# Performance work log

Hardware: AMD Instinct MI355X
Metric: run time of the kernel (lower is better)

## Reference

```python
import jax, jax.numpy as jnp
import numpy as np

PI = 3.141592653589793


def setup_inputs() -> dict:
    key = jax.random.key(0)
    k1, k2, k3, k4 = jax.random.split(key, 4)
    B, N, C, H, V = 4, 4096, 128, 8, 16
    inputs = jax.random.normal(k1, (B, N, C), dtype=jnp.float32)
    dist = jax.random.uniform(k2, (N, N), dtype=jnp.float32)
    r = jax.random.normal(k3, (H, 1, 1), dtype=jnp.float32)
    weight = jax.random.normal(k4, (H, C, V), dtype=jnp.float32)
    return {"inputs": inputs, "dist": dist, "r": r, "weight": weight, "locality": 64}


def reference(inputs, dist, r, weight, locality):
    # scaled_dist: (H, N, N) -- learnable bandwidth per head via tan/sin transform
    scaled = dist[None, :, :] * jnp.tan(0.25 * PI * (1.0 + jnp.sin(r)))
    # quantile-based local masking along last axis (linear interpolation,
    # matching tfp.stats.percentile with interpolation='linear')
    mask = jnp.percentile(scaled, float(locality), axis=-1, keepdims=True, method="linear")
    fmax = jnp.finfo(jnp.float32).max
    scaled = jnp.where(scaled <= mask, scaled, fmax)
    # softmax over key axis of -scaled_dist (masked entries -> -fmax -> ~0 weight)
    att = jax.nn.softmax(-scaled, axis=-1)  # (H, N, N)
    # per-head value projection: (B,N,C) x (H,C,V) -> (B,H,N,V)
    value = jnp.einsum("bnj,hjk->bhnk", inputs, weight)
    # attention aggregation: (H,N,N) x (B,H,N,V) -> (B,H,N,V)
    concat = jnp.einsum("hnj,bhjd->bhnd", att, value)
    B, H, N, V = concat.shape
    concat = concat.transpose(0, 2, 1, 3).reshape(B, N, H * V)  # (B, N, hid_dim)
    # tf.keras.activations.gelu defaults to exact (non-approximate) gelu
    return jax.nn.gelu(concat, approximate=False)
```

## Files before the change

### kernel.cpp

```cpp
#include <hip/hip_runtime.h>
#include <hip/hip_bf16.h>
#include <math.h>

#define NN 4096
#define NC 128
#define NH 8
#define NV 16
#define NB 4
#define BD 64

typedef _Float16 half8 __attribute__((ext_vector_type(8)));
typedef __fp16  fp16x2 __attribute__((ext_vector_type(2)));
typedef float floatx4 __attribute__((ext_vector_type(4)));

__device__ __forceinline__ int get_loc(const int* locp){
    int lr = locp[0];
    return (lr >= 0 && lr <= 100) ? lr : 64;
}
__device__ __forceinline__ float head_scale(const float* rr, int h){
    float ts = tanf(0.78539816339744831f * (1.0f + sinf(rr[h])));
    if (!(ts > 0.f)) ts = (ts == 0.f) ? 1e-20f : 1e20f;
    if (ts > 1e20f) ts = 1e20f;
    return ts;
}
__device__ __forceinline__ void lds_barrier(){
    __asm__ __volatile__("s_waitcnt lgkmcnt(0)\n\ts_barrier" ::: "memory");
}

__global__ __launch_bounds__(256) void k_prep(const float* __restrict__ dist,
                                              const int* __restrict__ locp,
                                              const float* __restrict__ in,
                                              const float* __restrict__ wgt,
                                              float* __restrict__ Kval,
                                              float* __restrict__ xminp,
                                              _Float16* __restrict__ val_t){
    __shared__ unsigned int hist[4][256];
    __shared__ float cand[1024];
    __shared__ unsigned int cnt, selb_s, basec_s, xminu;

    const int t = threadIdx.x, lane = t & 63, wv = t >> 6;

    if (blockIdx.x < 512){
        const int idx = blockIdx.x;
        const int b   = idx & 3;
        const int j0  = (idx >> 2) * 32;
        const int kl  = (lane >> 4) * 8;
        const int v   = lane & 15;

        half8 Bf[2][4];
#pragma unroll
        for (int nt = 0; nt < 2; nt++){
            const int h = wv * 2 + nt;
            const float* wp = wgt + ((size_t)h * NC + kl) * NV + v;
#pragma unroll
            for (int kc = 0; kc < 4; kc++)
#pragma unroll
                for (int u = 0; u < 8; u++)
                    Bf[nt][kc][u] = (_Float16)wp[(kc * 32 + u) * NV];
        }

        floatx4 acc[2][2];
#pragma unroll
        for (int a = 0; a < 2; a++)
#pragma unroll
            for (int c = 0; c < 2; c++) acc[a][c] = (floatx4){0.f,0.f,0.f,0.f};

        const float* ip = in + ((size_t)b * NN + j0 + v) * NC + kl;
#pragma unroll
        for (int jm = 0; jm < 2; jm++){
            const float* ipm = ip + jm * 16 * NC;
#pragma unroll
            for (int kc = 0; kc < 4; kc++){
                float4 x0 = *(const float4*)(ipm + kc * 32);
                float4 x1 = *(const float4*)(ipm + kc * 32 + 4);
                const float xs[8] = {x0.x,x0.y,x0.z,x0.w,x1.x,x1.y,x1.z,x1.w};
                union { half8 h8; fp16x2 h2[4]; } hi, lo;
#pragma unroll
                for (int u = 0; u < 4; u++){
                    hi.h2[u] = __builtin_amdgcn_cvt_pkrtz(xs[2*u], xs[2*u+1]);
                    float r0 = xs[2*u]   - (float)hi.h2[u][0];
                    float r1 = xs[2*u+1] - (float)hi.h2[u][1];
                    lo.h2[u] = __builtin_amdgcn_cvt_pkrtz(r0, r1);
                }
#pragma unroll
                for (int nt = 0; nt < 2; nt++){
                    acc[jm][nt] = __builtin_amdgcn_mfma_f32_16x16x32_f16(hi.h8, Bf[nt][kc], acc[jm][nt], 0, 0, 0);
                    acc[jm][nt] = __builtin_amdgcn_mfma_f32_16x16x32_f16(lo.h8, Bf[nt][kc], acc[jm][nt], 0, 0, 0);
                }
            }
        }

        const int jw = (lane >> 4) * 4;
#pragma unroll
        for (int jm = 0; jm < 2; jm++)
#pragma unroll
            for (int nt = 0; nt < 2; nt++){
                const int h   = wv * 2 + nt;
                const int row = h * BD + b * NV + v;
                union { _Float16 hh[4]; uint2 u; } o;
#pragma unroll
                for (int u = 0; u < 4; u++) o.hh[u] = (_Float16)acc[jm][nt][u];
                *(uint2*)&val_t[(size_t)row * NN + j0 + jm * 16 + jw] = o.u;
            }
        return;
    }

    const int i = blockIdx.x - 512;
    const int loc = get_loc(locp);
    const unsigned int rank = (unsigned int)(((long long)loc * (NN - 1)) / 100) + 1u;

    float v[16];
    const float4* rp = (const float4*)(dist + (size_t)i * NN);
#pragma unroll
    for (int k = 0; k < 4; k++){
        float4 x4 = rp[k * 256 + t];
        v[4*k+0] = x4.x; v[4*k+1] = x4.y; v[4*k+2] = x4.z; v[4*k+3] = x4.w;
    }
    for (int k = t; k < 1024; k += 256) ((unsigned int*)hist)[k] = 0;
    if (t == 0){ cnt = 0; selb_s = 255u; basec_s = 0u; xminu = 0xFFFFFFFFu; }
    __syncthreads();

    float lmin = 1e30f;
#pragma unroll
    for (int u = 0; u < 16; u++){
        float x = v[u];
        lmin = fminf(lmin, x);
        int b = (int)(x * 256.0f); b = b < 0 ? 0 : (b > 255 ? 255 : b);
        atomicAdd(&hist[wv][b], 1u);
    }
#pragma unroll
    for (int off = 1; off < 64; off <<= 1) lmin = fminf(lmin, __shfl_xor(lmin, off));
    if (lane == 0) atomicMin(&xminu, __float_as_uint(lmin));
    __syncthreads();

    if (t < 64){
        unsigned int lp[4];
        unsigned int run = 0;
#pragma unroll
        for (int q = 0; q < 4; q++){
            int b = 4 * t + q;
            run += hist[0][b] + hist[1][b] + hist[2][b] + hist[3][b];
            lp[q] = run;
        }
        unsigned int incl = run;
#pragma unroll
        for (int d = 1; d < 64; d <<= 1){
            unsigned int y = __shfl_up(incl, d);
            if (t >= d) incl += y;
        }
        unsigned int excl = incl - run;
        if (excl < rank && rank <= incl){
#pragma unroll
            for (int q = 0; q < 4; q++){
                if (excl + lp[q] >= rank){
                    selb_s  = (unsigned int)(4 * t + q);
                    basec_s = excl + (q ? lp[q-1] : 0u);
                    break;
                }
            }
        }
    }
    __syncthreads();
    const unsigned int sb = selb_s;
    if (t == 0) Kval[i] = ((float)sb + 1.0f) * 0.00390625f;
#pragma unroll
    for (int u = 0; u < 16; u++){
        float x = v[u];
        int b = (int)(x * 256.0f); b = b < 0 ? 0 : (b > 255 ? 255 : b);
        if ((unsigned int)b == sb){
            unsigned int idx = atomicAdd(&cnt, 1u);
            if (idx < 1024u) cand[idx] = x;
        }
    }
    __syncthreads();
    const unsigned int n = cnt > 1024u ? 1024u : cnt;
    const unsigned int need = rank - basec_s;
    for (unsigned int c0 = t; c0 < n; c0 += 256){
        float x = cand[c0];
        unsigned int lt = 0, le = 0;
        for (unsigned int k2 = 0; k2 < n; k2++){
            float y = cand[k2];
            lt += (y < x); le += (y <= x);
        }
        if (lt < need && need <= le) Kval[i] = x;
    }
    if (t == 0) xminp[i] = __uint_as_float(xminu);
}

__global__ __launch_bounds__(256) void k_att(const float* __restrict__ dist,
                                             const float* __restrict__ rr,
                                             const _Float16* __restrict__ val_t,
                                             const float* __restrict__ Kvalp,
                                             const float* __restrict__ xminp,
                                             float* __restrict__ out){
    __shared__ alignas(16) _Float16 wtile[2][32 * 72];
    __shared__ alignas(16) _Float16 vtile[2][64 * 72];

    const int l   = blockIdx.x + (NN / 32) * blockIdx.y;
    const int xcd = l & 7;
    const int s   = l >> 3;
    const int i0  = (xcd * 16 + (s >> 3)) * 32;
    const int h   = s & 7;

    const int t = threadIdx.x;
    const int lane = t & 63, wv = t >> 6;
    const float ts  = head_scale(rr, h);
    const float ts2 = ts * 1.44269504088896f;

    const int il = t >> 3, jq = t & 7;
    const int vrow = t >> 3, vpart = t & 7;
    const float kvi  = Kvalp[i0 + il];
    const float txmi = ts2 * xminp[i0 + il];
    const float nts2 = -ts2;

    half8 ones;
#pragma unroll
    for (int u = 0; u < 8; u++) ones[u] = (_Float16)1.0f;

    const float* dp = dist + (size_t)(i0 + il) * NN + jq * 8;
    const _Float16* vp0 = val_t + (size_t)(h * BD + vrow) * NN + vpart * 8;
    const _Float16* vp1 = vp0 + (size_t)32 * NN;

    floatx4 acc0 = (floatx4){0.f,0.f,0.f,0.f};
    floatx4 acc1 = (floatx4){0.f,0.f,0.f,0.f};
    floatx4 accs = (floatx4){0.f,0.f,0.f,0.f};

    const int is16 = (wv & 1) * 16;
    const int bh   = (wv >> 1) * 32;
    const int aoff  = (is16 + (lane & 15)) * 72 + (lane >> 4) * 8;
    const int boff0 = (bh + (lane & 15)) * 72 + (lane >> 4) * 8;
    const int boff1 = boff0 + 16 * 72;
    const int voff0 = vrow * 72 + vpart * 8;
    const int voff1 = (vrow + 32) * 72 + vpart * 8;
    const int woff  = il * 72 + jq * 8;

    uint4  Av0, Av1, Bv0, Bv1;
    float4 Ad0, Ad1, Bd0, Bd1;

#define LOADSET(V0, V1, D0, D1) do{                                          \
        V0 = *(const uint4*)vp0;  vp0 += 64;                                 \
        V1 = *(const uint4*)vp1;  vp1 += 64;                                 \
        D0 = *(const float4*)dp;                                             \
        D1 = *(const float4*)(dp + 4);  dp += 64; }while(0)

#define STAGE(BUF, V0, V1, D0, D1) do{                                       \
        *(uint4*)&vtile[BUF][voff0] = V0;                                    \
        *(uint4*)&vtile[BUF][voff1] = V1;                                    \
        const float dd_[8] = {D0.x,D0.y,D0.z,D0.w,D1.x,D1.y,D1.z,D1.w};      \
        union { half8 h8; fp16x2 h2[4]; } uu_;                               \
        _Pragma("unroll")                                                    \
        for (int u_ = 0; u_ < 4; u_++){                                      \
            float a0_ = fmaf(nts2, dd_[2*u_  ], txmi);                       \
            float a1_ = fmaf(nts2, dd_[2*u_+1], txmi);                       \
            a0_ = (dd_[2*u_  ] <= kvi) ? a0_ : -20000.0f;                    \
            a1_ = (dd_[2*u_+1] <= kvi) ? a1_ : -20000.0f;                    \
            uu_.h2[u_] = __builtin_amdgcn_cvt_pkrtz(                         \
                __builtin_amdgcn_exp2f(a0_), __builtin_amdgcn_exp2f(a1_));   \
        }                                                                    \
        *(half8*)&wtile[BUF][woff] = uu_.h8; }while(0)

#define MFMA_T(BUF) do{                                                      \
        _Pragma("unroll")                                                    \
        for (int kc_ = 0; kc_ < 2; kc_++){                                   \
            half8 af = *(const half8*)&wtile[BUF][aoff  + kc_ * 32];         \
            half8 b0 = *(const half8*)&vtile[BUF][boff0 + kc_ * 32];         \
            half8 b1 = *(const half8*)&vtile[BUF][boff1 + kc_ * 32];         \
            acc0 = __builtin_amdgcn_mfma_f32_16x16x32_f16(af, b0, acc0, 0, 0, 0); \
            acc1 = __builtin_amdgcn_mfma_f32_16x16x32_f16(af, b1, acc1, 0, 0, 0); \
            accs = __builtin_amdgcn_mfma_f32_16x16x32_f16(af, ones, accs, 0, 0, 0); \
        } }while(0)

    LOADSET(Av0, Av1, Ad0, Ad1);
    LOADSET(Bv0, Bv1, Bd0, Bd1);
    STAGE(0, Av0, Av1, Ad0, Ad1);

    for (int jp = 0; jp < 31; jp++){
        LOADSET(Av0, Av1, Ad0, Ad1);
        lds_barrier();
        MFMA_T(0);
        STAGE(1, Bv0, Bv1, Bd0, Bd1);
        LOADSET(Bv0, Bv1, Bd0, Bd1);
        lds_barrier();
        MFMA_T(1);
        STAGE(0, Av0, Av1, Ad0, Ad1);
    }
    lds_barrier();
    MFMA_T(0);
    STAGE(1, Bv0, Bv1, Bd0, Bd1);
    lds_barrier();
    MFMA_T(1);

#undef LOADSET
#undef STAGE
#undef MFMA_T

    const int m0 = (lane >> 4) * 4;
    const int d  = lane & 15;
#pragma unroll
    for (int r4 = 0; r4 < 4; r4++){
        const int iloc = is16 + m0 + r4;
        const float inv_s = 1.0f / fmaxf(accs[r4], 1e-30f);
#pragma unroll
        for (int nt = 0; nt < 2; nt++){
            const int b = (wv >> 1) * 2 + nt;
            float c = acc0[r4], c1 = acc1[r4];
            float cc = (nt == 0 ? c : c1) * inv_s;
            float g = 0.5f * cc * (1.0f + erff(cc * 0.70710678118654752f));
            out[((size_t)b * NN + i0 + iloc) * (NH * NV) + h * NV + d] = g;
        }
    }
}

extern "C" void kernel_launch(void* const* d_in, const int* in_sizes, int n_in,
                              void* d_out, int out_size, void* d_ws, size_t ws_size,
                              hipStream_t stream) {
    const float* in   = (const float*)d_in[0];
    const float* dist = (const float*)d_in[1];
    const float* r    = (const float*)d_in[2];
    const float* wgt  = (const float*)d_in[3];
    const int*   loc  = (const int*)d_in[4];
    float* out = (float*)d_out;

    float* Kval = (float*)d_ws;
    float* xmin = Kval + NN;
    _Float16* val_t = (_Float16*)((char*)d_ws + 2 * (size_t)NN * sizeof(float));

    k_prep<<<512 + NN, 256, 0, stream>>>(dist, loc, in, wgt, Kval, xmin, val_t);
    k_att<<<dim3(NN / 32, NH), 256, 0, stream>>>(dist, r, val_t, Kval, xmin, out);
}
```

Baseline: 168.5 us.

## Enlarge attention tile to 64 query rows with 512-thread blocks

The attention kernel now handles 64 query rows per block using 512 threads (8 waves) instead of 32 rows with 256 threads, and the grid shrinks from 1024 to 512 blocks. Each staged value tile (64 rows of V for the head) is reused across twice as many query rows, which halves redundant global loads of val_t and the per-thread value load/store work. The cost is more LDS per block, fewer blocks in flight, and a changed wave-to-tile mapping.

```diff
diff --git a/kernel.cpp b/kernel.cpp
--- a/kernel.cpp
+++ b/kernel.cpp
@@ -187,65 +187,60 @@
     if (t == 0) xminp[i] = __uint_as_float(xminu);
 }
 
-__global__ __launch_bounds__(256) void k_att(const float* __restrict__ dist,
+__global__ __launch_bounds__(512) void k_att(const float* __restrict__ dist,
                                              const float* __restrict__ rr,
                                              const _Float16* __restrict__ val_t,
                                              const float* __restrict__ Kvalp,
                                              const float* __restrict__ xminp,
                                              float* __restrict__ out){
-    __shared__ alignas(16) _Float16 wtile[2][32 * 72];
+    __shared__ alignas(16) _Float16 wtile[2][64 * 72];
     __shared__ alignas(16) _Float16 vtile[2][64 * 72];
 
-    const int l   = blockIdx.x + (NN / 32) * blockIdx.y;
+    const int l   = blockIdx.x;
     const int xcd = l & 7;
     const int s   = l >> 3;
-    const int i0  = (xcd * 16 + (s >> 3)) * 32;
+    const int i0  = (xcd * 8 + (s >> 3)) * 64;
     const int h   = s & 7;
 
     const int t = threadIdx.x;
     const int lane = t & 63, wv = t >> 6;
     const float ts  = head_scale(rr, h);
     const float ts2 = ts * 1.44269504088896f;
+    const float nts2 = -ts2;
 
     const int il = t >> 3, jq = t & 7;
-    const int vrow = t >> 3, vpart = t & 7;
     const float kvi  = Kvalp[i0 + il];
     const float txmi = ts2 * xminp[i0 + il];
-    const float nts2 = -ts2;
+
+    const float* dp = dist + (size_t)(i0 + il) * NN + jq * 8;
+    const _Float16* vp = val_t + (size_t)(h * BD + il) * NN + jq * 8;
 
     half8 ones;
 #pragma unroll
     for (int u = 0; u < 8; u++) ones[u] = (_Float16)1.0f;
-
-    const float* dp = dist + (size_t)(i0 + il) * NN + jq * 8;
-    const _Float16* vp0 = val_t + (size_t)(h * BD + vrow) * NN + vpart * 8;
-    const _Float16* vp1 = vp0 + (size_t)32 * NN;
 
     floatx4 acc0 = (floatx4){0.f,0.f,0.f,0.f};
     floatx4 acc1 = (floatx4){0.f,0.f,0.f,0.f};
     floatx4 accs = (floatx4){0.f,0.f,0.f,0.f};
 
-    const int is16 = (wv & 1) * 16;
-    const int bh   = (wv >> 1) * 32;
-    const int aoff  = (is16 + (lane & 15)) * 72 + (lane >> 4) * 8;
+    const int iq16 = (wv >> 1) * 16;
+    const int bh   = (wv & 1) * 32;
+    const int aoff  = (iq16 + (lane & 15)) * 72 + (lane >> 4) * 8;
     const int boff0 = (bh + (lane & 15)) * 72 + (lane >> 4) * 8;
     const int boff1 = boff0 + 16 * 72;
-    const int voff0 = vrow * 72 + vpart * 8;
-    const int voff1 = (vrow + 32) * 72 + vpart * 8;
-    const int woff  = il * 72 + jq * 8;
-
-    uint4  Av0, Av1, Bv0, Bv1;
+    const int voff  = il * 72 + jq * 8;
+    const int woff  = voff;
+
+    uint4  Av, Bv;
     float4 Ad0, Ad1, Bd0, Bd1;
 
-#define LOADSET(V0, V1, D0, D1) do{                                          \
-        V0 = *(const uint4*)vp0;  vp0 += 64;                                 \
-        V1 = *(const uint4*)vp1;  vp1 += 64;                                 \
+#define LOADSET(V, D0, D1) do{                                               \
+        V  = *(const uint4*)vp;  vp += 64;                                   \
         D0 = *(const float4*)dp;                                             \
         D1 = *(const float4*)(dp + 4);  dp += 64; }while(0)
 
-#define STAGE(BUF, V0, V1, D0, D1) do{                                       \
-        *(uint4*)&vtile[BUF][voff0] = V0;                                    \
-        *(uint4*)&vtile[BUF][voff1] = V1;                                    \
+#define STAGE(BUF, V, D0, D1) do{                                            \
+        *(uint4*)&vtile[BUF][voff] = V;                                      \
         const float dd_[8] = {D0.x,D0.y,D0.z,D0.w,D1.x,D1.y,D1.z,D1.w};      \
         union { half8 h8; fp16x2 h2[4]; } uu_;                               \
         _Pragma("unroll")                                                    \
@@ -270,23 +265,23 @@
             accs = __builtin_amdgcn_mfma_f32_16x16x32_f16(af, ones, accs, 0, 0, 0); \
         } }while(0)
 
-    LOADSET(Av0, Av1, Ad0, Ad1);
-    LOADSET(Bv0, Bv1, Bd0, Bd1);
-    STAGE(0, Av0, Av1, Ad0, Ad1);
+    LOADSET(Av, Ad0, Ad1);
+    LOADSET(Bv, Bd0, Bd1);
+    STAGE(0, Av, Ad0, Ad1);
 
     for (int jp = 0; jp < 31; jp++){
-        LOADSET(Av0, Av1, Ad0, Ad1);
+        LOADSET(Av, Ad0, Ad1);
         lds_barrier();
         MFMA_T(0);
-        STAGE(1, Bv0, Bv1, Bd0, Bd1);
-        LOADSET(Bv0, Bv1, Bd0, Bd1);
+        STAGE(1, Bv, Bd0, Bd1);
+        LOADSET(Bv, Bd0, Bd1);
         lds_barrier();
         MFMA_T(1);
-        STAGE(0, Av0, Av1, Ad0, Ad1);
+        STAGE(0, Av, Ad0, Ad1);
     }
     lds_barrier();
     MFMA_T(0);
-    STAGE(1, Bv0, Bv1, Bd0, Bd1);
+    STAGE(1, Bv, Bd0, Bd1);
     lds_barrier();
     MFMA_T(1);
 
@@ -298,15 +293,15 @@
     const int d  = lane & 15;
 #pragma unroll
     for (int r4 = 0; r4 < 4; r4++){
-        const int iloc = is16 + m0 + r4;
+        const int i = i0 + iq16 + m0 + r4;
         const float inv_s = 1.0f / fmaxf(accs[r4], 1e-30f);
 #pragma unroll
         for (int nt = 0; nt < 2; nt++){
-            const int b = (wv >> 1) * 2 + nt;
+            const int b = (wv & 1) * 2 + nt;
             float c = acc0[r4], c1 = acc1[r4];
             float cc = (nt == 0 ? c : c1) * inv_s;
             float g = 0.5f * cc * (1.0f + erff(cc * 0.70710678118654752f));
-            out[((size_t)b * NN + i0 + iloc) * (NH * NV) + h * NV + d] = g;
+            out[((size_t)b * NN + i) * (NH * NV) + h * NV + d] = g;
         }
     }
 }
@@ -326,5 +321,5 @@
     _Float16* val_t = (_Float16*)((char*)d_ws + 2 * (size_t)NN * sizeof(float));
 
     k_prep<<<512 + NN, 256, 0, stream>>>(dist, loc, in, wgt, Kval, xmin, val_t);
-    k_att<<<dim3(NN / 32, NH), 256, 0, stream>>>(dist, r, val_t, Kval, xmin, out);
-}
+    k_att<<<512, 512, 0, stream>>>(dist, r, val_t, Kval, xmin, out);
+}
```

Result: faster. 158.7 us (-5.9%).
